# Kernel tuning notes

Hardware: AMD Instinct MI355X
Metric: run time of the kernel (lower is better)

## Reference

```python
import jax, jax.numpy as jnp
import numpy as np

B, S, E, H = 2, 2048, 1024, 16
DH = E // H            # 64 head dim
ROT = DH // 2          # 32: RotaryEmbedding(head_dim//2) rotates first 32 dims only
CTX = 2048             # sliding KV window
THETA = 10000.0


def setup_inputs() -> dict:
    key = jax.random.key(0)
    ks = jax.random.split(key, 7)
    sc = 1.0 / np.sqrt(E)
    mk = lambda k, sh, s=1.0: (jax.random.normal(k, sh, jnp.float32) * s)
    return {
        "query": mk(ks[0], (B, S, E)),
        "key":   mk(ks[1], (B, S, E)),
        "value": mk(ks[2], (B, S, E)),
        "Wq": mk(ks[3], (E, E), sc), "bq": jnp.zeros((E,), jnp.float32),
        "Wk": mk(ks[4], (E, E), sc), "bk": jnp.zeros((E,), jnp.float32),
        "Wv": mk(ks[5], (E, E), sc), "bv": jnp.zeros((E,), jnp.float32),
        "Wo": mk(ks[6], (E, E), sc), "bo": jnp.zeros((E,), jnp.float32),
    }


def _rope(t):
    # t: [B, H, S, DH]; rotate first ROT dims, pass the rest through (offset=0).
    seq = t.shape[2]
    inv_freq = 1.0 / (THETA ** (jnp.arange(0, ROT, 2, dtype=jnp.float32) / ROT))  # [ROT//2]
    ang = jnp.arange(seq, dtype=jnp.float32)[:, None] * inv_freq[None, :]          # [S, ROT//2]
    cos = jnp.repeat(jnp.cos(ang), 2, axis=-1)  # [S, ROT] (pairwise-interleaved freqs)
    sin = jnp.repeat(jnp.sin(ang), 2, axis=-1)
    rot, rest = t[..., :ROT], t[..., ROT:]
    x1, x2 = rot[..., 0::2], rot[..., 1::2]
    rot_half = jnp.stack([-x2, x1], axis=-1).reshape(rot.shape)  # rotate_half on pairs
    return jnp.concatenate([rot * cos + rot_half * sin, rest], axis=-1)


def reference(query, key, value, Wq, bq, Wk, bk, Wv, bv, Wo, bo):
    def heads(x, W, b):
        return (x @ W.T + b).reshape(B, -1, H, DH).transpose(0, 2, 1, 3)  # [B,H,S,DH]

    q = _rope(heads(query, Wq, bq))
    k = _rope(heads(key, Wk, bk))
    v = heads(value, Wv, bv)
    k, v = k[:, :, -CTX:], v[:, :, -CTX:]  # sliding window (no-op when S == CTX)

    scale = jnp.float32(1.0 / np.sqrt(DH))
    scores = jnp.einsum('bhqd,bhkd->bhqk', q, k) * scale  # [B,H,Sq,Sk]
    sq, sk = q.shape[2], k.shape[2]
    causal = jnp.tril(jnp.ones((sk, sk), dtype=bool))[-sq:]  # [Sq,Sk]
    scores = jnp.where(causal[None, None], scores, jnp.float32(-jnp.inf))
    probs = jax.nn.softmax(scores, axis=-1)  # dropout=0 (eval)
    out = jnp.einsum('bhqk,bhkd->bhqd', probs, v)
    out = out.transpose(0, 2, 1, 3).reshape(B, -1, E)
    return out @ Wo.T + bo
```

## Files before the change

kernel.cpp:

```cpp
#include <hip/hip_runtime.h>
#include <stdint.h>
#include <math.h>

typedef __bf16 bf16x8 __attribute__((ext_vector_type(8)));
typedef float f32x4 __attribute__((ext_vector_type(4)));

__device__ __forceinline__ float bf2f(uint16_t x) {
  unsigned u = ((unsigned)x) << 16;
  float f;
  __builtin_memcpy(&f, &u, 4);
  return f;
}
__device__ __forceinline__ uint16_t f2bf(float f) {
  __bf16 h = (__bf16)f;
  uint16_t u;
  __builtin_memcpy(&u, &h, 2);
  return u;
}
__device__ __forceinline__ bf16x8 pack8(float4 lo, float4 hi) {
  bf16x8 v;
  v[0] = (__bf16)lo.x; v[1] = (__bf16)lo.y; v[2] = (__bf16)lo.z; v[3] = (__bf16)lo.w;
  v[4] = (__bf16)hi.x; v[5] = (__bf16)hi.y; v[6] = (__bf16)hi.z; v[7] = (__bf16)hi.w;
  return v;
}
__device__ __forceinline__ bf16x8 cvt8(const float* p) {
  return pack8(*(const float4*)p, *(const float4*)(p + 4));
}

typedef __attribute__((address_space(1))) const unsigned int gu32;
typedef __attribute__((address_space(3))) unsigned int lu32;
__device__ __forceinline__ void async_copy16(const void* gp, void* lp) {
  __builtin_amdgcn_global_load_lds((gu32*)gp, (lu32*)lp, 16, 0, 0);
}

__global__ __launch_bounds__(256) void cvt_kernel(
    const float* __restrict__ s0, uint16_t* __restrict__ d0,
    const float* __restrict__ s1, uint16_t* __restrict__ d1,
    const float* __restrict__ s2, uint16_t* __restrict__ d2,
    const float* __restrict__ s3, uint16_t* __restrict__ d3) {
  const int z = blockIdx.z;
  const float* s = z == 0 ? s0 : z == 1 ? s1 : z == 2 ? s2 : s3;
  uint16_t* d = z == 0 ? d0 : z == 1 ? d1 : z == 2 ? d2 : d3;
  const size_t idx = ((size_t)blockIdx.x * 256 + threadIdx.x) * 8;
  *(bf16x8*)(d + idx) = cvt8(s + idx);
}

template <bool A_F32, bool W_F32, bool C_F32, bool VT, bool ROPE, int BM, int NF>
__global__ __launch_bounds__(256) void gemm3_kernel(
    const void* __restrict__ A0, const void* __restrict__ W0,
    const float* __restrict__ b0, void* __restrict__ C0,
    const void* __restrict__ A1, const void* __restrict__ W1,
    const float* __restrict__ b1, void* __restrict__ C1,
    const void* __restrict__ A2, const void* __restrict__ W2,
    const float* __restrict__ b2, void* __restrict__ C2,
    int M, int N, int K) {
  constexpr int BN = NF * 32;
  constexpr int AF = BM / 32;
  const int z = blockIdx.z;
  const void* Av = z == 0 ? A0 : z == 1 ? A1 : A2;
  const void* Wp = z == 0 ? W0 : z == 1 ? W1 : W2;
  const float* bias = z == 0 ? b0 : z == 1 ? b1 : b2;
  void* Cv = z == 0 ? C0 : z == 1 ? C1 : C2;

  __shared__ __align__(16) uint16_t As[BM * 64];
  __shared__ __align__(16) uint16_t Bs[BN * 64];
  const int tid = threadIdx.x;
  const int wave = tid >> 6, lane = tid & 63;
  const int quad = lane >> 4, l16 = lane & 15;
  const int l = blockIdx.y * gridDim.x + blockIdx.x;
  const int nmt = M / BM;
  const int bm = (l % nmt) * BM;
  const int bn = (l / nmt) * BN;
  const int wm = (wave >> 1) * (BM / 2);
  const int wn = (wave & 1) * (BN / 2);

  f32x4 acc[AF][NF] = {};

  for (int k0 = 0; k0 < K; k0 += 64) {
    bf16x8 ar[AF], wr[NF];
    if (A_F32) {
#pragma unroll
      for (int i = 0; i < AF; i++) {
        const int c = i * 256 + tid;
        const int r = c >> 3, pc = ((c & 7) ^ (r & 7)) << 3;
        ar[i] = cvt8((const float*)Av + (size_t)(bm + r) * K + k0 + pc);
      }
    }
    if (W_F32) {
#pragma unroll
      for (int i = 0; i < NF; i++) {
        const int c = i * 256 + tid;
        const int r = c >> 3, pc = ((c & 7) ^ (r & 7)) << 3;
        wr[i] = cvt8((const float*)Wp + (size_t)(bn + r) * K + k0 + pc);
      }
    }
    if (k0) __syncthreads();
#pragma unroll
    for (int i = 0; i < AF; i++) {
      const int c = i * 256 + tid;
      const int r = c >> 3, pc = ((c & 7) ^ (r & 7)) << 3;
      if (A_F32) *(bf16x8*)(As + c * 8) = ar[i];
      else async_copy16((const uint16_t*)Av + (size_t)(bm + r) * K + k0 + pc,
                        As + (i * 256 + (tid & 192)) * 8);
    }
#pragma unroll
    for (int i = 0; i < NF; i++) {
      const int c = i * 256 + tid;
      const int r = c >> 3, pc = ((c & 7) ^ (r & 7)) << 3;
      if (W_F32) *(bf16x8*)(Bs + c * 8) = wr[i];
      else async_copy16((const uint16_t*)Wp + (size_t)(bn + r) * K + k0 + pc,
                        Bs + (i * 256 + (tid & 192)) * 8);
    }
    __syncthreads();
#pragma unroll
    for (int s = 0; s < 2; s++) {
      bf16x8 af[AF], bfr[NF];
#pragma unroll
      for (int i = 0; i < AF; i++) {
        const int Ra = wm + i * 16 + l16;
        af[i] = *(const bf16x8*)(As + Ra * 64 + (((s * 4 + quad) ^ (Ra & 7)) << 3));
      }
#pragma unroll
      for (int j = 0; j < NF; j++) {
        const int Rb = wn + j * 16 + l16;
        bfr[j] = *(const bf16x8*)(Bs + Rb * 64 + (((s * 4 + quad) ^ (Rb & 7)) << 3));
      }
#pragma unroll
      for (int i = 0; i < AF; i++)
#pragma unroll
        for (int j = 0; j < NF; j++)
          acc[i][j] = __builtin_amdgcn_mfma_f32_16x16x32_bf16(af[i], bfr[j], acc[i][j], 0, 0, 0);
    }
  }
  if (VT && z == 2) {
#pragma unroll
    for (int j = 0; j < NF; j++) {
      const int n = bn + wn + j * 16 + l16;
      const float bj = bias[n];
      const int h = n >> 6, dh = n & 63;
#pragma unroll
      for (int i = 0; i < AF; i++) {
        const int m0 = bm + wm + i * 16 + quad * 4;
        const int b = m0 >> 11, s0 = m0 & 2047;
        uint2 pk;
        pk.x = (unsigned)f2bf(acc[i][j][0] + bj) |
               ((unsigned)f2bf(acc[i][j][1] + bj) << 16);
        pk.y = (unsigned)f2bf(acc[i][j][2] + bj) |
               ((unsigned)f2bf(acc[i][j][3] + bj) << 16);
        *(uint2*)((uint16_t*)Cv + ((size_t)((b * 16 + h) * 64 + dh)) * 2048 + s0) = pk;
      }
    }
  } else {
#pragma unroll
    for (int j = 0; j < NF; j++) {
      const int n = bn + wn + j * 16 + l16;
      const float bj = bias[n];
      const int dh = (wn + j * 16 + l16) & 63;
      const bool rot = ROPE && (((wn + j * 16) & 63) < 32);
      float invrev = 0.f;
      if (rot)
        invrev = __expf(-0.5756462732485115f * (float)(dh >> 1)) *
                 0.15915494309189535f;
#pragma unroll
      for (int i = 0; i < AF; i++) {
        const int m0 = bm + wm + i * 16 + quad * 4;
#pragma unroll
        for (int r = 0; r < 4; r++) {
          float v = acc[i][j][r] + bj;
          if (rot) {
            const int s_pos = (m0 + r) & 2047;
            float rev = (float)s_pos * invrev;
            rev -= floorf(rev);
            const float sn = __builtin_amdgcn_sinf(rev);
            const float cs = __builtin_amdgcn_cosf(rev);
            const float partner = __shfl_xor(v, 1);
            v = (dh & 1) ? (v * cs + partner * sn) : (v * cs - partner * sn);
          }
          if (C_F32) ((float*)Cv)[(size_t)(m0 + r) * N + n] = v;
          else       ((uint16_t*)Cv)[(size_t)(m0 + r) * N + n] = f2bf(v);
        }
      }
    }
  }
}

__global__ __launch_bounds__(256) void flash_kernel(const uint16_t* __restrict__ Q,
                                                    const uint16_t* __restrict__ K,
                                                    const uint16_t* __restrict__ VT,
                                                    uint16_t* __restrict__ AO) {
  const int bx = blockIdx.x;
  const int xcd = bx & 7;
  const int slot = bx >> 3;
  const int bh = (slot >> 4) * 8 + xcd;
  const int qt2 = 15 - (slot & 15);
  const int h = bh & 15;
  const int b = bh >> 4;
  const int tid = threadIdx.x;
  const int wave = tid >> 6, lane = tid & 63;
  const int quad = lane >> 4, l16 = lane & 15;

  __shared__ __align__(16) uint16_t Ks[2][64 * 64];
  __shared__ __align__(16) uint16_t Vt[2][64 * 64];
  __shared__ __align__(16) uint16_t Ps[4][32 * 72];

  const int qrow0 = qt2 * 128 + wave * 16 + l16;
  const int qrow1 = qrow0 + 64;
  bf16x8 qf0[2], qf1[2];
#pragma unroll
  for (int s = 0; s < 2; s++) {
    union { bf16x8 v; uint16_t u[8]; } t0, t1;
    t0.v = *(const bf16x8*)(Q + ((size_t)(b * 2048 + qrow0) * 1024) + h * 64 + s * 32 + quad * 8);
    t1.v = *(const bf16x8*)(Q + ((size_t)(b * 2048 + qrow1) * 1024) + h * 64 + s * 32 + quad * 8);
#pragma unroll
    for (int j = 0; j < 8; j++) {
      t0.u[j] = f2bf(bf2f(t0.u[j]) * 0.125f);
      t1.u[j] = f2bf(bf2f(t1.u[j]) * 0.125f);
    }
    qf0[s] = t0.v;
    qf1[s] = t1.v;
  }

  const size_t vbase = ((size_t)((b * 16 + h) * 64)) * 2048;

  auto stage = [&](int buf, int kt) {
#pragma unroll
    for (int i = 0; i < 2; i++) {
      const int c = i * 256 + tid;
      const int r = c >> 3, pc = ((c & 7) ^ (r & 7)) << 3;
      async_copy16(K + ((size_t)(b * 2048 + kt * 64 + r) * 1024) + h * 64 + pc,
                   Ks[buf] + (i * 256 + (tid & 192)) * 8);
      async_copy16(VT + vbase + (size_t)r * 2048 + kt * 64 + pc,
                   Vt[buf] + (i * 256 + (tid & 192)) * 8);
    }
  };

  float lsum0 = 0.f, lsum1 = 0.f;
  f32x4 o0[4] = {}, o1[4] = {};

  const int nkt = 2 * qt2 + 2;
  stage(0, 0);
  __syncthreads();
  int cur = 0;
  for (int kt = 0; kt < nkt; kt++) {
    if (kt + 1 < nkt) stage(cur ^ 1, kt + 1);
    const uint16_t* ksp = Ks[cur];
    const uint16_t* vtp = Vt[cur];

    const bool f0 = (kt < nkt - 1);

    {
      f32x4 sacc[4] = {};
#pragma unroll
      for (int s = 0; s < 2; s++)
#pragma unroll
        for (int t = 0; t < 4; t++) {
          const int R = t * 16 + l16;
          bf16x8 kf = *(const bf16x8*)(ksp + R * 64 + (((s * 4 + quad) ^ (R & 7)) << 3));
          sacc[t] = __builtin_amdgcn_mfma_f32_16x16x32_bf16(kf, qf1[s], sacc[t], 0, 0, 0);
        }
      if (kt == nkt - 1) {
#pragma unroll
        for (int t = 0; t < 4; t++)
#pragma unroll
          for (int r = 0; r < 4; r++)
            if (kt * 64 + t * 16 + quad * 4 + r > qrow1) sacc[t][r] = -1e30f;
      }
#pragma unroll
      for (int t = 0; t < 4; t++) {
        float p0 = __expf(sacc[t][0]), p1 = __expf(sacc[t][1]);
        float p2 = __expf(sacc[t][2]), p3 = __expf(sacc[t][3]);
        lsum1 += (p0 + p1) + (p2 + p3);
        uint2 pk;
        pk.x = (unsigned)f2bf(p0) | ((unsigned)f2bf(p1) << 16);
        pk.y = (unsigned)f2bf(p2) | ((unsigned)f2bf(p3) << 16);
        *(uint2*)(&Ps[wave][(16 + l16) * 72 + t * 16 + quad * 4]) = pk;
      }
    }
    if (f0) {
      f32x4 sacc[4] = {};
#pragma unroll
      for (int s = 0; s < 2; s++)
#pragma unroll
        for (int t = 0; t < 4; t++) {
          const int R = t * 16 + l16;
          bf16x8 kf = *(const bf16x8*)(ksp + R * 64 + (((s * 4 + quad) ^ (R & 7)) << 3));
          sacc[t] = __builtin_amdgcn_mfma_f32_16x16x32_bf16(kf, qf0[s], sacc[t], 0, 0, 0);
        }
      if (kt == nkt - 2) {
#pragma unroll
        for (int t = 0; t < 4; t++)
#pragma unroll
          for (int r = 0; r < 4; r++)
            if (kt * 64 + t * 16 + quad * 4 + r > qrow0) sacc[t][r] = -1e30f;
      }
#pragma unroll
      for (int t = 0; t < 4; t++) {
        float p0 = __expf(sacc[t][0]), p1 = __expf(sacc[t][1]);
        float p2 = __expf(sacc[t][2]), p3 = __expf(sacc[t][3]);
        lsum0 += (p0 + p1) + (p2 + p3);
        uint2 pk;
        pk.x = (unsigned)f2bf(p0) | ((unsigned)f2bf(p1) << 16);
        pk.y = (unsigned)f2bf(p2) | ((unsigned)f2bf(p3) << 16);
        *(uint2*)(&Ps[wave][l16 * 72 + t * 16 + quad * 4]) = pk;
      }
    }
#pragma unroll
    for (int s = 0; s < 2; s++) {
      const bf16x8 pa1 = *(const bf16x8*)(&Ps[wave][(16 + l16) * 72 + s * 32 + quad * 8]);
#pragma unroll
      for (int t = 0; t < 4; t++) {
        const int R = t * 16 + l16;
        const bf16x8 vb = *(const bf16x8*)(vtp + R * 64 + (((s * 4 + quad) ^ (R & 7)) << 3));
        o1[t] = __builtin_amdgcn_mfma_f32_16x16x32_bf16(pa1, vb, o1[t], 0, 0, 0);
      }
    }
    if (f0) {
#pragma unroll
      for (int s = 0; s < 2; s++) {
        const bf16x8 pa0 = *(const bf16x8*)(&Ps[wave][l16 * 72 + s * 32 + quad * 8]);
#pragma unroll
        for (int t = 0; t < 4; t++) {
          const int R = t * 16 + l16;
          const bf16x8 vb = *(const bf16x8*)(vtp + R * 64 + (((s * 4 + quad) ^ (R & 7)) << 3));
          o0[t] = __builtin_amdgcn_mfma_f32_16x16x32_bf16(pa0, vb, o0[t], 0, 0, 0);
        }
      }
    }
    if (kt + 1 < nkt) {
      __syncthreads();
      cur ^= 1;
    }
  }
  lsum0 += __shfl_xor(lsum0, 16);
  lsum0 += __shfl_xor(lsum0, 32);
  lsum1 += __shfl_xor(lsum1, 16);
  lsum1 += __shfl_xor(lsum1, 32);
  const float inv0 = 1.f / lsum0, inv1 = 1.f / lsum1;
  float invr0[4], invr1[4];
#pragma unroll
  for (int r = 0; r < 4; r++) {
    invr0[r] = __shfl(inv0, quad * 4 + r);
    invr1[r] = __shfl(inv1, quad * 4 + r);
  }
#pragma unroll
  for (int t = 0; t < 4; t++)
#pragma unroll
    for (int r = 0; r < 4; r++) {
      const int qg0 = qt2 * 128 + wave * 16 + quad * 4 + r;
      AO[((size_t)(b * 2048 + qg0) * 1024) + h * 64 + t * 16 + l16] =
          f2bf(o0[t][r] * invr0[r]);
      AO[((size_t)(b * 2048 + qg0 + 64) * 1024) + h * 64 + t * 16 + l16] =
          f2bf(o1[t][r] * invr1[r]);
    }
}

extern "C" void kernel_launch(void* const* d_in, const int* in_sizes, int n_in,
                              void* d_out, int out_size, void* d_ws, size_t ws_size,
                              hipStream_t stream) {
  const float* query = (const float*)d_in[0];
  const float* key   = (const float*)d_in[1];
  const float* value = (const float*)d_in[2];
  const float* Wq = (const float*)d_in[3];
  const float* bq = (const float*)d_in[4];
  const float* Wk = (const float*)d_in[5];
  const float* bk = (const float*)d_in[6];
  const float* Wv = (const float*)d_in[7];
  const float* bv = (const float*)d_in[8];
  const float* Wo = (const float*)d_in[9];
  const float* bo = (const float*)d_in[10];
  float* out = (float*)d_out;

  uint16_t* ws = (uint16_t*)d_ws;
  uint16_t* Qb  = ws;
  uint16_t* Kb  = ws + (size_t)4194304;
  uint16_t* VTb = ws + (size_t)8388608;
  uint16_t* AOb = ws + (size_t)12582912;

  dim3 blk(256);

  if (ws_size >= (size_t)64 * 1024 * 1024) {
    uint16_t* Qc  = ws + (size_t)16777216;
    uint16_t* Kc  = ws + (size_t)20971520;
    uint16_t* Vc  = ws + (size_t)25165824;
    uint16_t* Wqc = ws + (size_t)29360128;
    uint16_t* Wkc = ws + (size_t)30408704;
    uint16_t* Wvc = ws + (size_t)31457280;
    uint16_t* Woc = ws + (size_t)32505856;

    cvt_kernel<<<dim3(512, 1, 4), blk, 0, stream>>>(
        Wq, Wqc, Wk, Wkc, Wv, Wvc, Wo, Woc);
    cvt_kernel<<<dim3(2048, 1, 3), blk, 0, stream>>>(
        query, Qc, key, Kc, value, Vc, nullptr, nullptr);
    gemm3_kernel<false, false, false, true, true, 128, 4><<<dim3(8, 32, 3), blk, 0, stream>>>(
        Qc, Wqc, bq, Qb,
        Kc, Wkc, bk, Kb,
        Vc, Wvc, bv, VTb,
        4096, 1024, 1024);
    flash_kernel<<<dim3(512), blk, 0, stream>>>(Qb, Kb, VTb, AOb);
    gemm3_kernel<false, false, true, false, false, 128, 2><<<dim3(16, 32, 1), blk, 0, stream>>>(
        AOb, Woc, bo, out,
        AOb, Woc, bo, out,
        AOb, Woc, bo, out,
        4096, 1024, 1024);
  } else {
    uint16_t* Wqc = AOb;
    uint16_t* Wkc = AOb + (size_t)1048576;
    uint16_t* Wvc = AOb + (size_t)2097152;
    cvt_kernel<<<dim3(512, 1, 3), blk, 0, stream>>>(
        Wq, Wqc, Wk, Wkc, Wv, Wvc, nullptr, nullptr);
    gemm3_kernel<true, false, false, true, true, 128, 2><<<dim3(16, 32, 3), blk, 0, stream>>>(
        query, Wqc, bq, Qb,
        key,   Wkc, bk, Kb,
        value, Wvc, bv, VTb,
        4096, 1024, 1024);
    flash_kernel<<<dim3(512), blk, 0, stream>>>(Qb, Kb, VTb, AOb);
    gemm3_kernel<false, true, true, false, false, 128, 2><<<dim3(16, 32, 1), blk, 0, stream>>>(
        AOb, Wo, bo, out,
        AOb, Wo, bo, out,
        AOb, Wo, bo, out,
        4096, 1024, 1024);
  }
}
```

Measured before the change: 230.4 us.

## Merge conversion launches, rebalance flash tile order, use exp2, stage KV in pairs

The two fp32-to-bf16 conversion launches become one kernel that converts activations and weights together, removing a launch. The flash kernel changes its query-tile mapping so the second half of the blocks runs in ascending order. It folds log2(e) into the Q scale so it can call the hardware exp2 directly. It also replaces the double-buffered one-tile prefetch with loading two KV tiles at once followed by a barrier. That halves the number of barriers but drops the overlap of loads with compute, and an odd tile count would load one tile past the causal range.

```diff
diff --git a/kernel.cpp b/kernel.cpp
--- a/kernel.cpp
+++ b/kernel.cpp
@@ -42,6 +42,31 @@
   const float* s = z == 0 ? s0 : z == 1 ? s1 : z == 2 ? s2 : s3;
   uint16_t* d = z == 0 ? d0 : z == 1 ? d1 : z == 2 ? d2 : d3;
   const size_t idx = ((size_t)blockIdx.x * 256 + threadIdx.x) * 8;
+  *(bf16x8*)(d + idx) = cvt8(s + idx);
+}
+
+__global__ __launch_bounds__(256) void cvt_all_kernel(
+    const float* __restrict__ q, uint16_t* __restrict__ qo,
+    const float* __restrict__ k, uint16_t* __restrict__ ko,
+    const float* __restrict__ v, uint16_t* __restrict__ vo,
+    const float* __restrict__ w0, uint16_t* __restrict__ w0o,
+    const float* __restrict__ w1, uint16_t* __restrict__ w1o,
+    const float* __restrict__ w2, uint16_t* __restrict__ w2o,
+    const float* __restrict__ w3, uint16_t* __restrict__ w3o) {
+  const int z = blockIdx.z;
+  const float* s;
+  uint16_t* d;
+  size_t idx;
+  if (z < 3) {
+    s = z == 0 ? q : z == 1 ? k : v;
+    d = z == 0 ? qo : z == 1 ? ko : vo;
+    idx = ((size_t)blockIdx.x * 256 + threadIdx.x) * 8;
+  } else {
+    const int w = blockIdx.x >> 9;
+    s = w == 0 ? w0 : w == 1 ? w1 : w == 2 ? w2 : w3;
+    d = w == 0 ? w0o : w == 1 ? w1o : w == 2 ? w2o : w3o;
+    idx = ((size_t)(blockIdx.x & 511) * 256 + threadIdx.x) * 8;
+  }
   *(bf16x8*)(d + idx) = cvt8(s + idx);
 }
 
@@ -192,7 +217,7 @@
   const int xcd = bx & 7;
   const int slot = bx >> 3;
   const int bh = (slot >> 4) * 8 + xcd;
-  const int qt2 = 15 - (slot & 15);
+  const int qt2 = (slot < 32) ? (15 - (slot & 15)) : (slot & 15);
   const int h = bh & 15;
   const int b = bh >> 4;
   const int tid = threadIdx.x;
@@ -203,6 +228,7 @@
   __shared__ __align__(16) uint16_t Vt[2][64 * 64];
   __shared__ __align__(16) uint16_t Ps[4][32 * 72];
 
+  const float QS = 0.18033688011112042f;
   const int qrow0 = qt2 * 128 + wave * 16 + l16;
   const int qrow1 = qrow0 + 64;
   bf16x8 qf0[2], qf1[2];
@@ -213,8 +239,8 @@
     t1.v = *(const bf16x8*)(Q + ((size_t)(b * 2048 + qrow1) * 1024) + h * 64 + s * 32 + quad * 8);
 #pragma unroll
     for (int j = 0; j < 8; j++) {
-      t0.u[j] = f2bf(bf2f(t0.u[j]) * 0.125f);
-      t1.u[j] = f2bf(bf2f(t1.u[j]) * 0.125f);
+      t0.u[j] = f2bf(bf2f(t0.u[j]) * QS);
+      t1.u[j] = f2bf(bf2f(t1.u[j]) * QS);
     }
     qf0[s] = t0.v;
     qf1[s] = t1.v;
@@ -222,113 +248,117 @@
 
   const size_t vbase = ((size_t)((b * 16 + h) * 64)) * 2048;
 
-  auto stage = [&](int buf, int kt) {
+  float lsum0 = 0.f, lsum1 = 0.f;
+  f32x4 o0[4] = {}, o1[4] = {};
+
+  const int nkt = 2 * qt2 + 2;
+  for (int outer = 0; outer < nkt; outer += 2) {
+    if (outer) __syncthreads();
 #pragma unroll
     for (int i = 0; i < 2; i++) {
       const int c = i * 256 + tid;
       const int r = c >> 3, pc = ((c & 7) ^ (r & 7)) << 3;
-      async_copy16(K + ((size_t)(b * 2048 + kt * 64 + r) * 1024) + h * 64 + pc,
-                   Ks[buf] + (i * 256 + (tid & 192)) * 8);
-      async_copy16(VT + vbase + (size_t)r * 2048 + kt * 64 + pc,
-                   Vt[buf] + (i * 256 + (tid & 192)) * 8);
-    }
-  };
-
-  float lsum0 = 0.f, lsum1 = 0.f;
-  f32x4 o0[4] = {}, o1[4] = {};
-
-  const int nkt = 2 * qt2 + 2;
-  stage(0, 0);
-  __syncthreads();
-  int cur = 0;
-  for (int kt = 0; kt < nkt; kt++) {
-    if (kt + 1 < nkt) stage(cur ^ 1, kt + 1);
-    const uint16_t* ksp = Ks[cur];
-    const uint16_t* vtp = Vt[cur];
-
-    const bool f0 = (kt < nkt - 1);
-
-    {
-      f32x4 sacc[4] = {};
-#pragma unroll
-      for (int s = 0; s < 2; s++)
+      const int ld = (i * 256 + (tid & 192)) * 8;
+#pragma unroll
+      for (int sub = 0; sub < 2; sub++) {
+        const int kt = outer + sub;
+        async_copy16(K + ((size_t)(b * 2048 + kt * 64 + r) * 1024) + h * 64 + pc,
+                     Ks[sub] + ld);
+        async_copy16(VT + vbase + (size_t)r * 2048 + kt * 64 + pc,
+                     Vt[sub] + ld);
+      }
+    }
+    __syncthreads();
+
+#pragma unroll
+    for (int sub = 0; sub < 2; sub++) {
+      const int kt = outer + sub;
+      const uint16_t* ksp = Ks[sub];
+      const uint16_t* vtp = Vt[sub];
+      const bool f0 = (kt < nkt - 1);
+
+      {
+        f32x4 sacc[4] = {};
+#pragma unroll
+        for (int s = 0; s < 2; s++)
+#pragma unroll
+          for (int t = 0; t < 4; t++) {
+            const int R = t * 16 + l16;
+            bf16x8 kf = *(const bf16x8*)(ksp + R * 64 + (((s * 4 + quad) ^ (R & 7)) << 3));
+            sacc[t] = __builtin_amdgcn_mfma_f32_16x16x32_bf16(kf, qf1[s], sacc[t], 0, 0, 0);
+          }
+        if (kt == nkt - 1) {
+#pragma unroll
+          for (int t = 0; t < 4; t++)
+#pragma unroll
+            for (int r = 0; r < 4; r++)
+              if (kt * 64 + t * 16 + quad * 4 + r > qrow1) sacc[t][r] = -1e30f;
+        }
 #pragma unroll
         for (int t = 0; t < 4; t++) {
-          const int R = t * 16 + l16;
-          bf16x8 kf = *(const bf16x8*)(ksp + R * 64 + (((s * 4 + quad) ^ (R & 7)) << 3));
-          sacc[t] = __builtin_amdgcn_mfma_f32_16x16x32_bf16(kf, qf1[s], sacc[t], 0, 0, 0);
-        }
-      if (kt == nkt - 1) {
-#pragma unroll
-        for (int t = 0; t < 4; t++)
-#pragma unroll
-          for (int r = 0; r < 4; r++)
-            if (kt * 64 + t * 16 + quad * 4 + r > qrow1) sacc[t][r] = -1e30f;
-      }
-#pragma unroll
-      for (int t = 0; t < 4; t++) {
-        float p0 = __expf(sacc[t][0]), p1 = __expf(sacc[t][1]);
-        float p2 = __expf(sacc[t][2]), p3 = __expf(sacc[t][3]);
-        lsum1 += (p0 + p1) + (p2 + p3);
-        uint2 pk;
-        pk.x = (unsigned)f2bf(p0) | ((unsigned)f2bf(p1) << 16);
-        pk.y = (unsigned)f2bf(p2) | ((unsigned)f2bf(p3) << 16);
-        *(uint2*)(&Ps[wave][(16 + l16) * 72 + t * 16 + quad * 4]) = pk;
-      }
-    }
-    if (f0) {
-      f32x4 sacc[4] = {};
-#pragma unroll
-      for (int s = 0; s < 2; s++)
+          float p0 = __builtin_amdgcn_exp2f(sacc[t][0]);
+          float p1 = __builtin_amdgcn_exp2f(sacc[t][1]);
+          float p2 = __builtin_amdgcn_exp2f(sacc[t][2]);
+          float p3 = __builtin_amdgcn_exp2f(sacc[t][3]);
+          lsum1 += (p0 + p1) + (p2 + p3);
+          uint2 pk;
+          pk.x = (unsigned)f2bf(p0) | ((unsigned)f2bf(p1) << 16);
+          pk.y = (unsigned)f2bf(p2) | ((unsigned)f2bf(p3) << 16);
+          *(uint2*)(&Ps[wave][(16 + l16) * 72 + t * 16 + quad * 4]) = pk;
+        }
+      }
+      if (f0) {
+        f32x4 sacc[4] = {};
+#pragma unroll
+        for (int s = 0; s < 2; s++)
+#pragma unroll
+          for (int t = 0; t < 4; t++) {
+            const int R = t * 16 + l16;
+            bf16x8 kf = *(const bf16x8*)(ksp + R * 64 + (((s * 4 + quad) ^ (R & 7)) << 3));
+            sacc[t] = __builtin_amdgcn_mfma_f32_16x16x32_bf16(kf, qf0[s], sacc[t], 0, 0, 0);
+          }
+        if (kt == nkt - 2) {
+#pragma unroll
+          for (int t = 0; t < 4; t++)
+#pragma unroll
+            for (int r = 0; r < 4; r++)
+              if (kt * 64 + t * 16 + quad * 4 + r > qrow0) sacc[t][r] = -1e30f;
+        }
 #pragma unroll
         for (int t = 0; t < 4; t++) {
-          const int R = t * 16 + l16;
-          bf16x8 kf = *(const bf16x8*)(ksp + R * 64 + (((s * 4 + quad) ^ (R & 7)) << 3));
-          sacc[t] = __builtin_amdgcn_mfma_f32_16x16x32_bf16(kf, qf0[s], sacc[t], 0, 0, 0);
-        }
-      if (kt == nkt - 2) {
-#pragma unroll
-        for (int t = 0; t < 4; t++)
-#pragma unroll
-          for (int r = 0; r < 4; r++)
-            if (kt * 64 + t * 16 + quad * 4 + r > qrow0) sacc[t][r] = -1e30f;
-      }
-#pragma unroll
-      for (int t = 0; t < 4; t++) {
-        float p0 = __expf(sacc[t][0]), p1 = __expf(sacc[t][1]);
-        float p2 = __expf(sacc[t][2]), p3 = __expf(sacc[t][3]);
-        lsum0 += (p0 + p1) + (p2 + p3);
-        uint2 pk;
-        pk.x = (unsigned)f2bf(p0) | ((unsigned)f2bf(p1) << 16);
-        pk.y = (unsigned)f2bf(p2) | ((unsigned)f2bf(p3) << 16);
-        *(uint2*)(&Ps[wave][l16 * 72 + t * 16 + quad * 4]) = pk;
-      }
-    }
-#pragma unroll
-    for (int s = 0; s < 2; s++) {
-      const bf16x8 pa1 = *(const bf16x8*)(&Ps[wave][(16 + l16) * 72 + s * 32 + quad * 8]);
-#pragma unroll
-      for (int t = 0; t < 4; t++) {
-        const int R = t * 16 + l16;
-        const bf16x8 vb = *(const bf16x8*)(vtp + R * 64 + (((s * 4 + quad) ^ (R & 7)) << 3));
-        o1[t] = __builtin_amdgcn_mfma_f32_16x16x32_bf16(pa1, vb, o1[t], 0, 0, 0);
-      }
-    }
-    if (f0) {
+          float p0 = __builtin_amdgcn_exp2f(sacc[t][0]);
+          float p1 = __builtin_amdgcn_exp2f(sacc[t][1]);
+          float p2 = __builtin_amdgcn_exp2f(sacc[t][2]);
+          float p3 = __builtin_amdgcn_exp2f(sacc[t][3]);
+          lsum0 += (p0 + p1) + (p2 + p3);
+          uint2 pk;
+          pk.x = (unsigned)f2bf(p0) | ((unsigned)f2bf(p1) << 16);
+          pk.y = (unsigned)f2bf(p2) | ((unsigned)f2bf(p3) << 16);
+          *(uint2*)(&Ps[wave][l16 * 72 + t * 16 + quad * 4]) = pk;
+        }
+      }
 #pragma unroll
       for (int s = 0; s < 2; s++) {
-        const bf16x8 pa0 = *(const bf16x8*)(&Ps[wave][l16 * 72 + s * 32 + quad * 8]);
+        const bf16x8 pa1 = *(const bf16x8*)(&Ps[wave][(16 + l16) * 72 + s * 32 + quad * 8]);
 #pragma unroll
         for (int t = 0; t < 4; t++) {
           const int R = t * 16 + l16;
           const bf16x8 vb = *(const bf16x8*)(vtp + R * 64 + (((s * 4 + quad) ^ (R & 7)) << 3));
-          o0[t] = __builtin_amdgcn_mfma_f32_16x16x32_bf16(pa0, vb, o0[t], 0, 0, 0);
-        }
-      }
-    }
-    if (kt + 1 < nkt) {
-      __syncthreads();
-      cur ^= 1;
+          o1[t] = __builtin_amdgcn_mfma_f32_16x16x32_bf16(pa1, vb, o1[t], 0, 0, 0);
+        }
+      }
+      if (f0) {
+#pragma unroll
+        for (int s = 0; s < 2; s++) {
+          const bf16x8 pa0 = *(const bf16x8*)(&Ps[wave][l16 * 72 + s * 32 + quad * 8]);
+#pragma unroll
+          for (int t = 0; t < 4; t++) {
+            const int R = t * 16 + l16;
+            const bf16x8 vb = *(const bf16x8*)(vtp + R * 64 + (((s * 4 + quad) ^ (R & 7)) << 3));
+            o0[t] = __builtin_amdgcn_mfma_f32_16x16x32_bf16(pa0, vb, o0[t], 0, 0, 0);
+          }
+        }
+      }
     }
   }
   lsum0 += __shfl_xor(lsum0, 16);
@@ -387,10 +417,9 @@
     uint16_t* Wvc = ws + (size_t)31457280;
     uint16_t* Woc = ws + (size_t)32505856;
 
-    cvt_kernel<<<dim3(512, 1, 4), blk, 0, stream>>>(
+    cvt_all_kernel<<<dim3(2048, 1, 4), blk, 0, stream>>>(
+        query, Qc, key, Kc, value, Vc,
         Wq, Wqc, Wk, Wkc, Wv, Wvc, Wo, Woc);
-    cvt_kernel<<<dim3(2048, 1, 3), blk, 0, stream>>>(
-        query, Qc, key, Kc, value, Vc, nullptr, nullptr);
     gemm3_kernel<false, false, false, true, true, 128, 4><<<dim3(8, 32, 3), blk, 0, stream>>>(
         Qc, Wqc, bq, Qb,
         Kc, Wkc, bk, Kb,
```

Result: faster. 216.6 us (-6.0%).
